# Kernel optimization log

Hardware: AMD Instinct MI355X
Metric: run time of the kernel (lower is better)

## Reference

```python
import jax, jax.numpy as jnp
import numpy as np

N_HEADS = 16


def setup_inputs() -> dict:
    key = jax.random.key(0)
    ks = jax.random.split(key, 5)
    B, S, D = 2, 2048, 1024
    H = N_HEADS
    return {
        "queries": jax.random.normal(ks[0], (B, S, D), dtype=jnp.float32),
        "keys": jax.random.normal(ks[1], (B, S, D), dtype=jnp.float32),
        "values": jax.random.normal(ks[2], (B, S, D), dtype=jnp.float32),
        "bias": jax.random.normal(ks[3], (1, H, S, S), dtype=jnp.float32) * 0.02,
        "w_out": jax.random.normal(ks[4], (D, D), dtype=jnp.float32) * (1.0 / np.sqrt(D)),
    }


def _split_heads(x, n_heads):
    B, S, D = x.shape
    return x.reshape(B, S, n_heads, D // n_heads).transpose(0, 2, 1, 3)  # [B,H,S,hd]


def reference(queries, keys, values, bias, w_out):
    H = N_HEADS
    q = _split_heads(queries, H)
    k = _split_heads(keys, H)
    v = _split_heads(values, H)
    hd = k.shape[-1]
    # NOTE: original adds bias to raw logits, THEN scales by 1/sqrt(dk)
    logits = jnp.einsum("bhqd,bhkd->bhqk", q, k) + bias
    weights = jax.nn.softmax(logits * (1.0 / np.sqrt(hd)), axis=-1)
    attn = jnp.einsum("bhqk,bhkd->bhqd", weights, v)  # [B,H,Sq,hd]
    B, _, Sq, _ = attn.shape
    combined = attn.transpose(0, 2, 1, 3).reshape(B, Sq, H * hd)
    return combined @ w_out
```

## Files before the change

### kernel.cpp

```cpp
#include <hip/hip_runtime.h>

typedef float  f32x4  __attribute__((ext_vector_type(4)));
typedef short  bf16x8 __attribute__((ext_vector_type(8)));
typedef short  s16x4  __attribute__((ext_vector_type(4)));
typedef unsigned int u32x4 __attribute__((ext_vector_type(4)));

#define MFMA_BF16 __builtin_amdgcn_mfma_f32_16x16x32_bf16

__device__ __forceinline__ short f2bf(float f) {
  __bf16 h = (__bf16)f;
  return __builtin_bit_cast(short, h);
}

constexpr int S = 2048, D = 1024, H = 16, HD = 64;
constexpr int NT = S / 64;
constexpr int NTH = 16;
constexpr float SCALE = 0.125f;
constexpr float L2E = 1.44269504f;
constexpr float SL = SCALE * L2E;

#define GLDS16(g, l) __builtin_amdgcn_global_load_lds( \
    (const __attribute__((address_space(1))) unsigned*)(g), \
    (__attribute__((address_space(3))) unsigned*)(l), 16, 0, 0)

#define WAITV(n) asm volatile("s_waitcnt vmcnt(" #n ")" ::: "memory")
#define SBAR()   __builtin_amdgcn_s_barrier()

__global__ __launch_bounds__(256)
void kv_prep(const float* __restrict__ Kg, const float* __restrict__ Vg,
             short* __restrict__ KVb) {
  const int tile = blockIdx.x, h = blockIdx.y, b = blockIdx.z;
  const int t = threadIdx.x, lane = t & 63, w = t >> 6;
  const int lg = lane >> 4, lm = lane & 15;
  __shared__ short kt[64 * 68], vt[64 * 68];
  const float* kp = Kg + ((size_t)(b * S + tile * 64)) * D + h * HD;
  const float* vp = Vg + ((size_t)(b * S + tile * 64)) * D + h * HD;
  #pragma unroll
  for (int i = 0; i < 4; ++i) {
    int idx = i * 256 + t, r = idx >> 4, c4 = (idx & 15) * 4;
    float4 k4 = *(const float4*)(kp + (size_t)r * D + c4);
    s16x4 ks; ks[0]=f2bf(k4.x); ks[1]=f2bf(k4.y); ks[2]=f2bf(k4.z); ks[3]=f2bf(k4.w);
    *(s16x4*)&kt[r * 68 + c4] = ks;
    float4 v4 = *(const float4*)(vp + (size_t)r * D + c4);
    s16x4 vs; vs[0]=f2bf(v4.x); vs[1]=f2bf(v4.y); vs[2]=f2bf(v4.z); vs[3]=f2bf(v4.w);
    *(s16x4*)&vt[r * 68 + c4] = vs;
  }
  __syncthreads();
  const size_t obase = ((size_t)((b * H + h) * NT + tile)) * 8192;
  #pragma unroll
  for (int j = 0; j < 2; ++j) {
    int f = w + j * 4, kk = f >> 2, mf = f & 3;
    int row = mf * 16 + lm, col = kk * 32 + lg * 4;
    s16x4 c0 = *(const s16x4*)&kt[row * 68 + col];
    s16x4 c1 = *(const s16x4*)&kt[row * 68 + col + 16];
    bf16x8 a;
    a[0]=c0[0]; a[1]=c0[1]; a[2]=c0[2]; a[3]=c0[3];
    a[4]=c1[0]; a[5]=c1[1]; a[6]=c1[2]; a[7]=c1[3];
    *(bf16x8*)&KVb[obase + (size_t)(f * 64 + lane) * 8] = a;
  }
  #pragma unroll
  for (int j = 0; j < 2; ++j) {
    int fv = w + j * 4, kk = fv >> 2, of = fv & 3;
    int col = of * 16 + lm;
    bf16x8 a;
    #pragma unroll
    for (int half = 0; half < 2; ++half)
      #pragma unroll
      for (int e = 0; e < 4; ++e)
        a[half * 4 + e] = vt[(kk * 32 + lg * 4 + half * 16 + e) * 68 + col];
    *(bf16x8*)&KVb[obase + (size_t)((8 + fv) * 64 + lane) * 8] = a;
  }
}

__global__ __launch_bounds__(256, 3)
void attn_fused(const float* __restrict__ Qg, const float* __restrict__ Bg,
                const short* __restrict__ KVb,
                float* __restrict__ OP, float* __restrict__ ML) {
  __shared__ __attribute__((aligned(16))) short smem[16384];
  const int bid = blockIdx.x;
  const int c = bid & 7, g = bid >> 3;
  const int qb = g & 15, z = g >> 4;
  const int h = (c << 1) | (z & 1);
  const int b = (z >> 1) & 1;
  const int half = z >> 2;
  const int q0 = qb * 128;
  const int t = threadIdx.x, lane = t & 63, w = t >> 6;
  const int lg = lane >> 4, lm = lane & 15;

  bf16x8 qf[2][2];
  #pragma unroll
  for (int fq = 0; fq < 2; ++fq) {
    const float* qp = Qg + ((size_t)(b * S + q0 + w * 32 + fq * 16 + lm)) * D + h * HD;
    #pragma unroll
    for (int kk = 0; kk < 2; ++kk)
      #pragma unroll
      for (int j = 0; j < 8; ++j)
        qf[fq][kk][j] = f2bf(qp[kk * 32 + (j >> 2) * 16 + lg * 4 + (j & 3)]);
  }

  const short* KVt = KVb + ((size_t)((b * H + h) * NT + half * NTH)) * 8192;
  const float* bp = Bg + ((size_t)(h * S + q0 + w * 32 + lm)) * S + half * 1024 + lg * 4;

  const f32x4 zero4 = {0.f, 0.f, 0.f, 0.f};
  f32x4 o[2][4];
  #pragma unroll
  for (int fq = 0; fq < 2; ++fq)
    #pragma unroll
    for (int i = 0; i < 4; ++i) o[fq][i] = zero4;
  float M[2] = {-__builtin_inff(), -__builtin_inff()};
  float L[2] = {0.f, 0.f};
  f32x4 sacc[2][4];

#define STAGE(tile, buf)                                                \
  {                                                                     \
    const short* kvg_ = KVt + (size_t)(tile) * 8192;                    \
    _Pragma("unroll")                                                   \
    for (int f_ = 0; f_ < 4; ++f_) {                                    \
      int fr_ = w * 4 + f_;                                             \
      GLDS16(kvg_ + (size_t)(fr_ * 64 + lane) * 8, (buf) + fr_ * 512);  \
    }                                                                   \
  }

#define BLOAD(tile)                                                     \
  {                                                                     \
    _Pragma("unroll")                                                   \
    for (int fq_ = 0; fq_ < 2; ++fq_)                                   \
      _Pragma("unroll")                                                 \
      for (int mf_ = 0; mf_ < 4; ++mf_)                                 \
        sacc[fq_][mf_] = *(const f32x4*)(bp + (size_t)fq_ * 16 * S +    \
                                         (size_t)(tile) * 64 + mf_ * 16); \
  }

  STAGE(0, smem);
  BLOAD(0);

  for (int tt = 0; tt < NTH; ++tt) {
    SBAR();
    if (tt < NTH - 1) {
      STAGE(tt + 1, smem + ((tt + 1) & 1) * 8192);
      WAITV(12);
    } else {
      WAITV(8);
    }
    SBAR();
    const short* buf = smem + (tt & 1) * 8192;

    __builtin_amdgcn_s_setprio(1);
    #pragma unroll
    for (int kk = 0; kk < 2; ++kk)
      #pragma unroll
      for (int mf = 0; mf < 4; ++mf) {
        bf16x8 a = *(const bf16x8*)&buf[(kk * 4 + mf) * 512 + lane * 8];
        sacc[0][mf] = MFMA_BF16(a, qf[0][kk], sacc[0][mf], 0, 0, 0);
        sacc[1][mf] = MFMA_BF16(a, qf[1][kk], sacc[1][mf], 0, 0, 0);
      }
    __builtin_amdgcn_s_setprio(0);

    float tmax[2] = {-__builtin_inff(), -__builtin_inff()};
    #pragma unroll
    for (int fq = 0; fq < 2; ++fq)
      #pragma unroll
      for (int mf = 0; mf < 4; ++mf)
        #pragma unroll
        for (int j = 0; j < 4; ++j) {
          float tv = sacc[fq][mf][j] * SL;
          sacc[fq][mf][j] = tv;
          tmax[fq] = fmaxf(tmax[fq], tv);
        }
    #pragma unroll
    for (int fq = 0; fq < 2; ++fq) {
      tmax[fq] = fmaxf(tmax[fq], __shfl_xor(tmax[fq], 16, 64));
      tmax[fq] = fmaxf(tmax[fq], __shfl_xor(tmax[fq], 32, 64));
    }
    const int skip = (tmax[0] <= M[0]) && (tmax[1] <= M[1]);
    if (!__all(skip)) {
      #pragma unroll
      for (int fq = 0; fq < 2; ++fq) {
        float Mn = fmaxf(M[fq], tmax[fq]);
        float alpha = exp2f(M[fq] - Mn);
        #pragma unroll
        for (int of = 0; of < 4; ++of) {
          o[fq][of][0] *= alpha; o[fq][of][1] *= alpha;
          o[fq][of][2] *= alpha; o[fq][of][3] *= alpha;
        }
        L[fq] *= alpha;
        M[fq] = Mn;
      }
    }
    #pragma unroll
    for (int fq = 0; fq < 2; ++fq) {
      float psum = 0.f;
      #pragma unroll
      for (int mf = 0; mf < 4; ++mf)
        #pragma unroll
        for (int j = 0; j < 4; ++j) {
          float e = exp2f(sacc[fq][mf][j] - M[fq]);
          sacc[fq][mf][j] = e;
          psum += e;
        }
      psum += __shfl_xor(psum, 16, 64);
      psum += __shfl_xor(psum, 32, 64);
      L[fq] += psum;
    }
    bf16x8 pb[2][2];
    #pragma unroll
    for (int fq = 0; fq < 2; ++fq)
      #pragma unroll
      for (int kk = 0; kk < 2; ++kk)
        #pragma unroll
        for (int j = 0; j < 8; ++j)
          pb[fq][kk][j] = f2bf(sacc[fq][kk * 2 + (j >> 2)][j & 3]);

    if (tt < NTH - 1) BLOAD(tt + 1);

    __builtin_amdgcn_s_setprio(1);
    #pragma unroll
    for (int kk = 0; kk < 2; ++kk)
      #pragma unroll
      for (int of = 0; of < 4; ++of) {
        bf16x8 a = *(const bf16x8*)&buf[4096 + (kk * 4 + of) * 512 + lane * 8];
        o[0][of] = MFMA_BF16(a, pb[0][kk], o[0][of], 0, 0, 0);
        o[1][of] = MFMA_BF16(a, pb[1][kk], o[1][of], 0, 0, 0);
      }
    __builtin_amdgcn_s_setprio(0);
  }

  const int p = ((b * H + h) << 4) | qb;
  float* opb = OP + ((size_t)(half * 512 + p)) * 8192;
  #pragma unroll
  for (int fq = 0; fq < 2; ++fq)
    #pragma unroll
    for (int of = 0; of < 4; ++of)
      *(f32x4*)&opb[(w * 32 + fq * 16 + lm) * 64 + of * 16 + lg * 4] = o[fq][of];
  float* mlb = ML + ((size_t)(half * 512 + p)) * 256;
  if (lane < 16) {
    mlb[w * 32 + lm]        = M[0];
    mlb[w * 32 + 16 + lm]   = M[1];
    mlb[128 + w * 32 + lm]      = L[0];
    mlb[128 + w * 32 + 16 + lm] = L[1];
  }
#undef STAGE
#undef BLOAD
}

__global__ __launch_bounds__(256)
void combine(const float* __restrict__ OP, const float* __restrict__ ML,
             short* __restrict__ comb) {
  const int p = blockIdx.x;
  const int b = p >> 8, h = (p >> 4) & 15, qb = p & 15;
  const int t = threadIdx.x;
  const float* o1 = OP + (size_t)p * 8192;
  const float* o2 = OP + (size_t)(512 + p) * 8192;
  const float* m1p = ML + (size_t)p * 256;
  const float* m2p = ML + (size_t)(512 + p) * 256;
  #pragma unroll
  for (int k = 0; k < 8; ++k) {
    int e = (k * 256 + t) * 4;
    int q = e >> 6, d = e & 63;
    f32x4 a = *(const f32x4*)&o1[e];
    f32x4 c = *(const f32x4*)&o2[e];
    float m1 = m1p[q], m2 = m2p[q];
    float l1 = m1p[128 + q], l2 = m2p[128 + q];
    float m = fmaxf(m1, m2);
    float a1 = exp2f(m1 - m), a2 = exp2f(m2 - m);
    float inv = 1.f / (l1 * a1 + l2 * a2);
    s16x4 r;
    #pragma unroll
    for (int j = 0; j < 4; ++j)
      r[j] = f2bf((a[j] * a1 + c[j] * a2) * inv);
    *(s16x4*)&comb[((size_t)(b * S + qb * 128 + q)) * D + h * HD + d] = r;
  }
}

__global__ __launch_bounds__(256)
void wt_kernel(const float* __restrict__ W, short* __restrict__ Wt) {
  __shared__ __attribute__((aligned(16))) short tile[64 * 72];
  const int n0 = blockIdx.x * 64, k0 = blockIdx.y * 64;
  const int t = threadIdx.x;
  #pragma unroll
  for (int i = 0; i < 4; ++i) {
    int idx = i * 256 + t;
    int r  = idx >> 4, c4 = (idx & 15) * 4;
    float4 wv = *(const float4*)(W + (size_t)(k0 + r) * D + n0 + c4);
    tile[(c4 + 0) * 72 + r] = f2bf(wv.x);
    tile[(c4 + 1) * 72 + r] = f2bf(wv.y);
    tile[(c4 + 2) * 72 + r] = f2bf(wv.z);
    tile[(c4 + 3) * 72 + r] = f2bf(wv.w);
  }
  __syncthreads();
  #pragma unroll
  for (int it = 0; it < 2; ++it) {
    int idx = it * 256 + t;
    int r = idx >> 3, seg = idx & 7;
    u32x4 u = *(const u32x4*)&tile[r * 72 + seg * 8];
    *(u32x4*)&Wt[(size_t)(n0 + r) * D + k0 + seg * 8] = u;
  }
}

__device__ __forceinline__ bf16x8 ld_frag_swz(const short* base, int row, int kk, int lg) {
  const char* rp = (const char*)base + row * 128 + (lg & 1) * 8;
  int u0 = kk * 4 + (lg >> 1);
  int f  = row & 7;
  s16x4 c0 = *(const s16x4*)(rp + ((u0 ^ f) << 4));
  s16x4 c1 = *(const s16x4*)(rp + (((u0 + 2) ^ f) << 4));
  bf16x8 a;
  a[0]=c0[0]; a[1]=c0[1]; a[2]=c0[2]; a[3]=c0[3];
  a[4]=c1[0]; a[5]=c1[1]; a[6]=c1[2]; a[7]=c1[3];
  return a;
}

__global__ __launch_bounds__(256, 2)
void proj_gemm(const short* __restrict__ A, const short* __restrict__ Bt,
               float* __restrict__ C) {
  __shared__ __attribute__((aligned(16))) short a_lds[2][8192];
  __shared__ __attribute__((aligned(16))) short b_lds[2][4096];
  const int m0 = blockIdx.x * 128, n0 = blockIdx.y * 64;
  const int t = threadIdx.x, lane = t & 63, w = t >> 6;
  const int lg = lane >> 4, lm = lane & 15;
  const int srow = lane >> 3;
  const int sunit = (lane & 7) ^ srow;

  const f32x4 zero4 = {0.f, 0.f, 0.f, 0.f};
  f32x4 acc[2][4];
  #pragma unroll
  for (int i = 0; i < 2; ++i)
    #pragma unroll
    for (int j = 0; j < 4; ++j) acc[i][j] = zero4;

#define PSTAGE(ks, ab, bb)                                                  \
  {                                                                         \
    const short* ag_ = A  + (size_t)m0 * D + (ks) * 64;                     \
    const short* bg_ = Bt + (size_t)n0 * D + (ks) * 64;                     \
    _Pragma("unroll")                                                       \
    for (int i_ = 0; i_ < 4; ++i_) {                                        \
      int j_ = w * 4 + i_;                                                  \
      GLDS16(ag_ + (size_t)(j_ * 8 + srow) * D + sunit * 8, (ab) + j_ * 512); \
    }                                                                       \
    _Pragma("unroll")                                                       \
    for (int i_ = 0; i_ < 2; ++i_) {                                        \
      int j_ = w * 2 + i_;                                                  \
      GLDS16(bg_ + (size_t)(j_ * 8 + srow) * D + sunit * 8, (bb) + j_ * 512); \
    }                                                                       \
  }

#define PCOMPUTE(ab, bb)                                                    \
  {                                                                         \
    _Pragma("unroll")                                                       \
    for (int kk = 0; kk < 2; ++kk) {                                        \
      bf16x8 af0 = ld_frag_swz(ab, w * 32 + lm, kk, lg);                    \
      bf16x8 af1 = ld_frag_swz(ab, w * 32 + 16 + lm, kk, lg);               \
      bf16x8 bf0 = ld_frag_swz(bb, lm, kk, lg);                             \
      bf16x8 bf1 = ld_frag_swz(bb, 16 + lm, kk, lg);                        \
      bf16x8 bf2 = ld_frag_swz(bb, 32 + lm, kk, lg);                        \
      bf16x8 bf3 = ld_frag_swz(bb, 48 + lm, kk, lg);                        \
      __builtin_amdgcn_s_setprio(1);                                        \
      acc[0][0] = MFMA_BF16(af0, bf0, acc[0][0], 0, 0, 0);                  \
      acc[0][1] = MFMA_BF16(af0, bf1, acc[0][1], 0, 0, 0);                  \
      acc[0][2] = MFMA_BF16(af0, bf2, acc[0][2], 0, 0, 0);                  \
      acc[0][3] = MFMA_BF16(af0, bf3, acc[0][3], 0, 0, 0);                  \
      acc[1][0] = MFMA_BF16(af1, bf0, acc[1][0], 0, 0, 0);                  \
      acc[1][1] = MFMA_BF16(af1, bf1, acc[1][1], 0, 0, 0);                  \
      acc[1][2] = MFMA_BF16(af1, bf2, acc[1][2], 0, 0, 0);                  \
      acc[1][3] = MFMA_BF16(af1, bf3, acc[1][3], 0, 0, 0);                  \
      __builtin_amdgcn_s_setprio(0);                                        \
    }                                                                       \
  }

  PSTAGE(0, a_lds[0], b_lds[0]);
  for (int ks = 0; ks < 16; ks += 2) {
    SBAR();
    PSTAGE(ks + 1, a_lds[1], b_lds[1]);
    WAITV(6);
    SBAR();
    PCOMPUTE(a_lds[0], b_lds[0]);
    SBAR();
    if (ks + 2 < 16) {
      PSTAGE(ks + 2, a_lds[0], b_lds[0]);
      WAITV(6);
    } else {
      WAITV(0);
    }
    SBAR();
    PCOMPUTE(a_lds[1], b_lds[1]);
  }

  #pragma unroll
  for (int mf = 0; mf < 2; ++mf)
    #pragma unroll
    for (int j = 0; j < 4; ++j)
      #pragma unroll
      for (int nf = 0; nf < 4; ++nf)
        C[(size_t)(m0 + w * 32 + mf * 16 + lg * 4 + j) * D +
          n0 + nf * 16 + lm] = acc[mf][nf][j];
#undef PSTAGE
#undef PCOMPUTE
}

extern "C" void kernel_launch(void* const* d_in, const int* in_sizes, int n_in,
                              void* d_out, int out_size, void* d_ws, size_t ws_size,
                              hipStream_t stream) {
  const float* Qg = (const float*)d_in[0];
  const float* Kg = (const float*)d_in[1];
  const float* Vg = (const float*)d_in[2];
  const float* Bg = (const float*)d_in[3];
  const float* Wg = (const float*)d_in[4];
  float* out = (float*)d_out;

  short* comb = (short*)d_ws;
  short* Wt   = comb + (size_t)4096 * 1024;
  short* KVb  = Wt   + (size_t)1024 * 1024;
  float* OP   = (float*)(KVb + (size_t)2 * H * NT * 8192);
  float* ML   = OP + (size_t)2 * 512 * 8192;

  kv_prep<<<dim3(NT, H, 2), 256, 0, stream>>>(Kg, Vg, KVb);
  wt_kernel<<<dim3(D / 64, D / 64), 256, 0, stream>>>(Wg, Wt);
  attn_fused<<<dim3(1024), 256, 0, stream>>>(Qg, Bg, KVb, OP, ML);
  combine<<<dim3(512), 256, 0, stream>>>(OP, ML, comb);
  proj_gemm<<<dim3(32, 16), 256, 0, stream>>>(comb, Wt, out);
}
```

Baseline: 168.4 us.

## Double attention block query tile to 256 rows with 512 threads sharing KV tiles

The attention kernel now runs 8 waves per block covering 256 query rows instead of 4 waves over 128, so each staged K/V tile in LDS is reused by twice as many queries and each wave issues half as many async loads. The grid is halved to 512 blocks and the launch bound targets 4 blocks of 512 threads per CU. The partial-output layout becomes fragment-native, and the combine kernel is rewritten to read it, merge the two halves, and transpose through LDS so global writes are coalesced. The cost is fewer blocks in the grid, a higher register budget per block, and an extra LDS round-trip in combine.

```diff
diff --git a/kernel.cpp b/kernel.cpp
--- a/kernel.cpp
+++ b/kernel.cpp
@@ -14,7 +14,7 @@
 
 constexpr int S = 2048, D = 1024, H = 16, HD = 64;
 constexpr int NT = S / 64;
-constexpr int NTH = 16;
+constexpr int NTH = NT / 2;
 constexpr float SCALE = 0.125f;
 constexpr float L2E = 1.44269504f;
 constexpr float SL = SCALE * L2E;
@@ -72,18 +72,18 @@
   }
 }
 
-__global__ __launch_bounds__(256, 3)
+__global__ __launch_bounds__(512, 4)
 void attn_fused(const float* __restrict__ Qg, const float* __restrict__ Bg,
                 const short* __restrict__ KVb,
                 float* __restrict__ OP, float* __restrict__ ML) {
   __shared__ __attribute__((aligned(16))) short smem[16384];
   const int bid = blockIdx.x;
   const int c = bid & 7, g = bid >> 3;
-  const int qb = g & 15, z = g >> 4;
+  const int qb = g & 7, z = g >> 3;
   const int h = (c << 1) | (z & 1);
   const int b = (z >> 1) & 1;
   const int half = z >> 2;
-  const int q0 = qb * 128;
+  const int q0 = qb * 256;
   const int t = threadIdx.x, lane = t & 63, w = t >> 6;
   const int lg = lane >> 4, lm = lane & 15;
 
@@ -99,7 +99,7 @@
   }
 
   const short* KVt = KVb + ((size_t)((b * H + h) * NT + half * NTH)) * 8192;
-  const float* bp = Bg + ((size_t)(h * S + q0 + w * 32 + lm)) * S + half * 1024 + lg * 4;
+  const float* bp = Bg + ((size_t)(h * S + q0 + w * 32 + lm)) * S + half * (NTH * 64) + lg * 4;
 
   const f32x4 zero4 = {0.f, 0.f, 0.f, 0.f};
   f32x4 o[2][4];
@@ -115,8 +115,8 @@
   {                                                                     \
     const short* kvg_ = KVt + (size_t)(tile) * 8192;                    \
     _Pragma("unroll")                                                   \
-    for (int f_ = 0; f_ < 4; ++f_) {                                    \
-      int fr_ = w * 4 + f_;                                             \
+    for (int f_ = 0; f_ < 2; ++f_) {                                    \
+      int fr_ = w * 2 + f_;                                             \
       GLDS16(kvg_ + (size_t)(fr_ * 64 + lane) * 8, (buf) + fr_ * 512);  \
     }                                                                   \
   }
@@ -138,7 +138,7 @@
     SBAR();
     if (tt < NTH - 1) {
       STAGE(tt + 1, smem + ((tt + 1) & 1) * 8192);
-      WAITV(12);
+      WAITV(10);
     } else {
       WAITV(8);
     }
@@ -225,19 +225,19 @@
     __builtin_amdgcn_s_setprio(0);
   }
 
-  const int p = ((b * H + h) << 4) | qb;
-  float* opb = OP + ((size_t)(half * 512 + p)) * 8192;
+  const int p = ((b * H + h) << 3) | qb;
+  float* opb = OP + ((size_t)(half * 256 + p)) * 16384 + w * 2048;
   #pragma unroll
   for (int fq = 0; fq < 2; ++fq)
     #pragma unroll
     for (int of = 0; of < 4; ++of)
-      *(f32x4*)&opb[(w * 32 + fq * 16 + lm) * 64 + of * 16 + lg * 4] = o[fq][of];
-  float* mlb = ML + ((size_t)(half * 512 + p)) * 256;
+      *(f32x4*)&opb[(fq * 4 + of) * 256 + lane * 4] = o[fq][of];
+  float* mlb = ML + ((size_t)(half * 256 + p)) * 512;
   if (lane < 16) {
     mlb[w * 32 + lm]        = M[0];
     mlb[w * 32 + 16 + lm]   = M[1];
-    mlb[128 + w * 32 + lm]      = L[0];
-    mlb[128 + w * 32 + 16 + lm] = L[1];
+    mlb[256 + w * 32 + lm]      = L[0];
+    mlb[256 + w * 32 + 16 + lm] = L[1];
   }
 #undef STAGE
 #undef BLOAD
@@ -246,30 +246,36 @@
 __global__ __launch_bounds__(256)
 void combine(const float* __restrict__ OP, const float* __restrict__ ML,
              short* __restrict__ comb) {
-  const int p = blockIdx.x;
-  const int b = p >> 8, h = (p >> 4) & 15, qb = p & 15;
-  const int t = threadIdx.x;
-  const float* o1 = OP + (size_t)p * 8192;
-  const float* o2 = OP + (size_t)(512 + p) * 8192;
-  const float* m1p = ML + (size_t)p * 256;
-  const float* m2p = ML + (size_t)(512 + p) * 256;
-  #pragma unroll
-  for (int k = 0; k < 8; ++k) {
-    int e = (k * 256 + t) * 4;
-    int q = e >> 6, d = e & 63;
-    f32x4 a = *(const f32x4*)&o1[e];
-    f32x4 c = *(const f32x4*)&o2[e];
-    float m1 = m1p[q], m2 = m2p[q];
-    float l1 = m1p[128 + q], l2 = m2p[128 + q];
-    float m = fmaxf(m1, m2);
-    float a1 = exp2f(m1 - m), a2 = exp2f(m2 - m);
-    float inv = 1.f / (l1 * a1 + l2 * a2);
+  const int w = blockIdx.x & 7, p = blockIdx.x >> 3;
+  const int b = p >> 7, h = (p >> 3) & 15, qb = p & 7;
+  const int t = threadIdx.x, lane = t & 63, fr2 = t >> 6;
+  __shared__ __attribute__((aligned(16))) short tile[32 * 72];
+  const float* op0 = OP + (size_t)p * 16384 + w * 2048;
+  const float* op1 = OP + (size_t)(256 + p) * 16384 + w * 2048;
+  const float* ml0 = ML + (size_t)p * 512;
+  const float* ml1 = ML + (size_t)(256 + p) * 512;
+  #pragma unroll
+  for (int ff = 0; ff < 2; ++ff) {
+    int f = fr2 + ff * 4, fq = f >> 2, of = f & 3;
+    int ql = fq * 16 + (lane & 15);
+    int d  = of * 16 + (lane >> 4) * 4;
+    float m0 = ml0[w * 32 + ql], m1 = ml1[w * 32 + ql];
+    float l0 = ml0[256 + w * 32 + ql], l1 = ml1[256 + w * 32 + ql];
+    float m = fmaxf(m0, m1);
+    float a0 = exp2f(m0 - m), a1 = exp2f(m1 - m);
+    float inv = 1.f / (l0 * a0 + l1 * a1);
+    f32x4 v0 = *(const f32x4*)&op0[f * 256 + lane * 4];
+    f32x4 v1 = *(const f32x4*)&op1[f * 256 + lane * 4];
     s16x4 r;
     #pragma unroll
     for (int j = 0; j < 4; ++j)
-      r[j] = f2bf((a[j] * a1 + c[j] * a2) * inv);
-    *(s16x4*)&comb[((size_t)(b * S + qb * 128 + q)) * D + h * HD + d] = r;
-  }
+      r[j] = f2bf((v0[j] * a0 + v1[j] * a1) * inv);
+    *(s16x4*)&tile[ql * 72 + d] = r;
+  }
+  __syncthreads();
+  const int row = t >> 3, seg = t & 7;
+  u32x4 u = *(const u32x4*)&tile[row * 72 + seg * 8];
+  *(u32x4*)&comb[((size_t)(b * S + qb * 256 + w * 32 + row)) * D + h * HD + seg * 8] = u;
 }
 
 __global__ __launch_bounds__(256)
@@ -410,11 +416,11 @@
   short* Wt   = comb + (size_t)4096 * 1024;
   short* KVb  = Wt   + (size_t)1024 * 1024;
   float* OP   = (float*)(KVb + (size_t)2 * H * NT * 8192);
-  float* ML   = OP + (size_t)2 * 512 * 8192;
+  float* ML   = OP + (size_t)2 * 256 * 16384;
 
   kv_prep<<<dim3(NT, H, 2), 256, 0, stream>>>(Kg, Vg, KVb);
   wt_kernel<<<dim3(D / 64, D / 64), 256, 0, stream>>>(Wg, Wt);
-  attn_fused<<<dim3(1024), 256, 0, stream>>>(Qg, Bg, KVb, OP, ML);
-  combine<<<dim3(512), 256, 0, stream>>>(OP, ML, comb);
+  attn_fused<<<dim3(512), 512, 0, stream>>>(Qg, Bg, KVb, OP, ML);
+  combine<<<dim3(2048), 256, 0, stream>>>(OP, ML, comb);
   proj_gemm<<<dim3(32, 16), 256, 0, stream>>>(comb, Wt, out);
 }
```

Measured after the change: 149.8 us, median of 2. -11.0%, faster.
